# Optimization experiments

Measured on AMD Instinct MI355X. Metric: run time of the kernel, lower is better.

Reference implementation:

```python
import jax, jax.numpy as jnp
import numpy as np

D = 8
W = 256
NUM_FREQS = 10
NUM_FREQS_VIEWS = 4
SKIPS = (4,)
PE_DIM = 3 + 2 * 3 * NUM_FREQS        # 63
VE_DIM = 3 + 2 * 3 * NUM_FREQS_VIEWS  # 27
N_RAYS, N_SAMPLES = 4096, 64


def embed(x, num_freqs):
    # torch order: [x, sin(x*f0), cos(x*f0), sin(x*f1), cos(x*f1), ...]
    freqs = (2.0 ** jnp.arange(num_freqs)).astype(x.dtype)
    xf = x[..., None, :] * freqs[:, None]              # [..., F, 3]
    sc = jnp.stack([jnp.sin(xf), jnp.cos(xf)], axis=-2)  # [..., F, 2, 3]
    return jnp.concatenate([x, sc.reshape(*x.shape[:-1], num_freqs * 6)], -1)


def setup_inputs() -> dict:
    key = jax.random.key(0)
    ks = iter(jax.random.split(key, 32))
    inp = {}
    inp["input_pts"] = jax.random.normal(next(ks), (N_RAYS, N_SAMPLES, 3), jnp.float32)
    inp["input_views"] = jax.random.normal(next(ks), (N_RAYS, 3), jnp.float32)
    # pts MLP: layer 5 (index 5) takes W + PE_DIM due to skip after layer 4
    in_dims = [PE_DIM] + [(W + PE_DIM) if i in SKIPS else W for i in range(D - 1)]
    for i, d in enumerate(in_dims):
        inp[f"pts_w{i}"] = jax.random.normal(next(ks), (d, W), jnp.float32) / np.sqrt(d).astype(np.float32)
        inp[f"pts_b{i}"] = jnp.zeros((W,), jnp.float32)
    inp["views_w"] = jax.random.normal(next(ks), (VE_DIM + W, W // 2), jnp.float32) / np.sqrt(VE_DIM + W).astype(np.float32)
    inp["views_b"] = jnp.zeros((W // 2,), jnp.float32)
    inp["feat_w"] = jax.random.normal(next(ks), (W, W), jnp.float32) / np.sqrt(W).astype(np.float32)
    inp["feat_b"] = jnp.zeros((W,), jnp.float32)
    inp["alpha_w"] = jax.random.normal(next(ks), (W, 1), jnp.float32) / np.sqrt(W).astype(np.float32)
    inp["alpha_b"] = jnp.zeros((1,), jnp.float32)
    inp["rgb_w"] = jax.random.normal(next(ks), (W // 2, 3), jnp.float32) / np.sqrt(W // 2).astype(np.float32)
    inp["rgb_b"] = jnp.zeros((3,), jnp.float32)
    return inp


def reference(input_pts, input_views,
              pts_w0, pts_b0, pts_w1, pts_b1, pts_w2, pts_b2, pts_w3, pts_b3,
              pts_w4, pts_b4, pts_w5, pts_b5, pts_w6, pts_b6, pts_w7, pts_b7,
              views_w, views_b, feat_w, feat_b, alpha_w, alpha_b, rgb_w, rgb_b):
    pts_ws = [pts_w0, pts_w1, pts_w2, pts_w3, pts_w4, pts_w5, pts_w6, pts_w7]
    pts_bs = [pts_b0, pts_b1, pts_b2, pts_b3, pts_b4, pts_b5, pts_b6, pts_b7]
    R, S = input_pts.shape[0], input_pts.shape[1]
    ep = embed(input_pts, NUM_FREQS).reshape(-1, PE_DIM)            # [R*S, 63]
    ev = embed(input_views, NUM_FREQS_VIEWS)                        # [R, 27]
    ev = jnp.broadcast_to(ev[:, None, :], (R, S, VE_DIM)).reshape(-1, VE_DIM)
    h = ep
    for i in range(D):
        h = jax.nn.relu(h @ pts_ws[i] + pts_bs[i])
        if i in SKIPS:
            h = jnp.concatenate([ep, h], -1)
    alpha = h @ alpha_w + alpha_b                                    # [R*S, 1]
    feature = h @ feat_w + feat_b                                    # [R*S, W]
    h2 = jax.nn.relu(jnp.concatenate([feature, ev], -1) @ views_w + views_b)
    rgb = h2 @ rgb_w + rgb_b                                         # [R*S, 3]
    return jnp.concatenate([rgb, alpha], -1).reshape(R, S, 4)
```

## Files before the change

kernel.cpp:

```cpp
#include <hip/hip_runtime.h>

typedef _Float16 h16;
typedef __attribute__((ext_vector_type(8))) _Float16 half8;
typedef __attribute__((ext_vector_type(4))) _Float16 half4;
typedef __attribute__((ext_vector_type(4))) float f32x4;
typedef __attribute__((ext_vector_type(16))) float f32x16;

#define LDH 264
#define LDE 72

constexpr size_t OFF_P0 = 0;
constexpr size_t OFF_P1 = 16384;
constexpr size_t OFF_P2 = 81920;
constexpr size_t OFF_P3 = 147456;
constexpr size_t OFF_P4 = 212992;
constexpr size_t OFF_P5 = 278528;
constexpr size_t OFF_P6 = 360448;
constexpr size_t OFF_P7 = 425984;
constexpr size_t OFF_FEAT = 491520;
constexpr size_t OFF_VIEWS = 557056;

__device__ __forceinline__ f32x16 mfma32(half8 a, half8 b, f32x16 c) {
  return __builtin_amdgcn_mfma_f32_32x32x16_f16(a, b, c, 0, 0, 0);
}

__global__ void convw_kernel(const float* __restrict__ src, h16* __restrict__ dst,
                             int Ksrc, int N, int Kp, int p, int npad) {
  int t = blockIdx.x * 256 + threadIdx.x;
  int nfrags = (Kp >> 4) * (N >> 5);
  int frag = t >> 6;
  if (frag >= nfrags) return;
  int l = t & 63;
  int ntiles = N >> 5;
  int kt = frag / ntiles;
  int nt = frag - kt * ntiles;
  int col = nt * 32 + (l & 31);
  int kbase = kt * 16 + (l >> 5) * 8;
  half8 v;
#pragma unroll
  for (int j = 0; j < 8; ++j) {
    int k = kbase + j;
    float x = 0.f;
    if (k < p) {
      x = src[(size_t)k * N + col];
    } else if (k >= p + npad) {
      int r = k - npad;
      if (r < Ksrc) x = src[(size_t)r * N + col];
    }
    v[j] = (h16)x;
  }
  *(half8*)(dst + (size_t)frag * 512 + (size_t)l * 8) = v;
}

struct Params {
  const float* pts;
  const float* views;
  const h16* wf;
  const float* pb[8];
  const float* views_b;
  const float* feat_b;
  const float* alpha_w;
  const float* alpha_b;
  const float* rgb_w;
  const float* rgb_b;
  float* out;
};

template <int KT, int KT0, bool RELU, bool PRE_BAR>
__device__ __forceinline__ void gemm256(const h16* __restrict__ src0, int ld0,
                                        const h16* __restrict__ src1, int ld1,
                                        const h16* __restrict__ wf,
                                        const float* __restrict__ bias,
                                        h16* __restrict__ dst,
                                        int w, int l) {
  const int lr = l & 31;
  const int lk = (l >> 5) * 8;
  f32x16 acc[2];
  acc[0] = (f32x16)0.f;
  acc[1] = (f32x16)0.f;

#pragma unroll
  for (int kt = 0; kt < KT; ++kt) {
    half8 a[2];
#pragma unroll
    for (int mt = 0; mt < 2; ++mt) {
      const h16* ap;
      if (kt < KT0) ap = src0 + (size_t)(mt * 32 + lr) * ld0 + kt * 16 + lk;
      else          ap = src1 + (size_t)(mt * 32 + lr) * ld1 + (kt - KT0) * 16 + lk;
      a[mt] = *(const half8*)ap;
    }
    half8 b = *(const half8*)(wf + ((size_t)(kt * 8 + w) * 64 + l) * 8);
#pragma unroll
    for (int mt = 0; mt < 2; ++mt)
      acc[mt] = mfma32(b, a[mt], acc[mt]);
  }
  if (PRE_BAR) __syncthreads();
#pragma unroll
  for (int mt = 0; mt < 2; ++mt) {
    int row = mt * 32 + lr;
#pragma unroll
    for (int g = 0; g < 4; ++g) {
      int n0 = w * 32 + g * 8 + (l >> 5) * 4;
      f32x4 bv = *(const f32x4*)(bias + n0);
      half4 pk;
#pragma unroll
      for (int i = 0; i < 4; ++i) {
        float v = acc[mt][g * 4 + i] + bv[i];
        if (RELU) v = fmaxf(v, 0.f);
        pk[i] = (h16)v;
      }
      *(half4*)(dst + (size_t)row * LDH + n0) = pk;
    }
  }
  __syncthreads();
}

__global__ __launch_bounds__(512, 4) void nerf_kernel(Params P) {
  __shared__ __align__(16) h16 ep[64 * LDE];
  __shared__ __align__(16) h16 h[64 * LDH];
  __shared__ __align__(16) h16 evp[32];
  __shared__ float alpha_s[64];

  const int tid = threadIdx.x;
  const int w = tid >> 6, l = tid & 63;
  const int lr = l & 31;
  const int lk = (l >> 5) * 8;
  const int ray = blockIdx.x;

  if (tid < 64) {
    const int s = tid;
    const float x0 = P.pts[((size_t)ray * 64 + s) * 3 + 0];
    const float x1 = P.pts[((size_t)ray * 64 + s) * 3 + 1];
    const float x2 = P.pts[((size_t)ray * 64 + s) * 3 + 2];
    h16* e = ep + (size_t)s * LDE;
    e[0] = (h16)x0; e[1] = (h16)x1; e[2] = (h16)x2;
#pragma unroll
    for (int f = 0; f < 10; ++f) {
      const float sc = (float)(1 << f);
      e[3 + 6 * f + 0] = (h16)sinf(x0 * sc);
      e[3 + 6 * f + 1] = (h16)sinf(x1 * sc);
      e[3 + 6 * f + 2] = (h16)sinf(x2 * sc);
      e[3 + 6 * f + 3] = (h16)cosf(x0 * sc);
      e[3 + 6 * f + 4] = (h16)cosf(x1 * sc);
      e[3 + 6 * f + 5] = (h16)cosf(x2 * sc);
    }
    e[63] = (h16)0.f;
  } else if (tid < 96) {
    const int idx = tid - 64;
    float v = 0.f;
    if (idx < 27) {
      if (idx < 3) {
        v = P.views[(size_t)ray * 3 + idx];
      } else {
        const int f = (idx - 3) / 6, rem = (idx - 3) % 6, d = rem % 3;
        const float x = P.views[(size_t)ray * 3 + d] * (float)(1 << f);
        v = (rem < 3) ? sinf(x) : cosf(x);
      }
    }
    evp[idx] = (h16)v;
  }
  __syncthreads();

  gemm256<4, 4, true, false>(ep, LDE, ep, LDE, P.wf + OFF_P0, P.pb[0], h, w, l);
  gemm256<16, 0, true, true>(ep, LDE, h, LDH, P.wf + OFF_P1, P.pb[1], h, w, l);
  gemm256<16, 0, true, true>(ep, LDE, h, LDH, P.wf + OFF_P2, P.pb[2], h, w, l);
  gemm256<16, 0, true, true>(ep, LDE, h, LDH, P.wf + OFF_P3, P.pb[3], h, w, l);
  gemm256<16, 0, true, true>(ep, LDE, h, LDH, P.wf + OFF_P4, P.pb[4], h, w, l);
  gemm256<20, 4, true, true>(ep, LDE, h, LDH, P.wf + OFF_P5, P.pb[5], h, w, l);
  gemm256<16, 0, true, true>(ep, LDE, h, LDH, P.wf + OFF_P6, P.pb[6], h, w, l);
  gemm256<16, 0, true, true>(ep, LDE, h, LDH, P.wf + OFF_P7, P.pb[7], h, w, l);

  if (tid < 256) {
    const int s = tid >> 2, q = tid & 3;
    float sum = 0.f;
#pragma unroll 8
    for (int k = 0; k < 64; ++k)
      sum += (float)h[(size_t)s * LDH + q * 64 + k] * P.alpha_w[q * 64 + k];
    sum += __shfl_xor(sum, 1);
    sum += __shfl_xor(sum, 2);
    if (q == 0) alpha_s[s] = sum + P.alpha_b[0];
  }

  gemm256<16, 0, false, true>(ep, LDE, h, LDH, P.wf + OFF_FEAT, P.feat_b, h, w, l);

  {
    f32x16 acc[2];
    acc[0] = (f32x16)0.f;
    acc[1] = (f32x16)0.f;
    if (w < 4) {
#pragma unroll
      for (int kt = 0; kt < 18; ++kt) {
        half8 a[2];
        if (kt < 16) {
#pragma unroll
          for (int mt = 0; mt < 2; ++mt)
            a[mt] = *(const half8*)(h + (size_t)(mt * 32 + lr) * LDH + kt * 16 + lk);
        } else {
          half8 av = *(const half8*)(evp + (kt - 16) * 16 + lk);
          a[0] = av; a[1] = av;
        }
        half8 b = *(const half8*)(P.wf + OFF_VIEWS + ((size_t)(kt * 4 + w) * 64 + l) * 8);
#pragma unroll
        for (int mt = 0; mt < 2; ++mt)
          acc[mt] = mfma32(b, a[mt], acc[mt]);
      }
    }
    __syncthreads();
    if (w < 4) {
#pragma unroll
      for (int mt = 0; mt < 2; ++mt) {
        int row = mt * 32 + lr;
#pragma unroll
        for (int g = 0; g < 4; ++g) {
          int n0 = w * 32 + g * 8 + (l >> 5) * 4;
          f32x4 bv = *(const f32x4*)(P.views_b + n0);
          half4 pk;
#pragma unroll
          for (int i = 0; i < 4; ++i)
            pk[i] = (h16)fmaxf(acc[mt][g * 4 + i] + bv[i], 0.f);
          *(half4*)(h + (size_t)row * LDH + n0) = pk;
        }
      }
    }
    __syncthreads();
  }

  if (tid < 256) {
    const int s = tid >> 2, q = tid & 3;
    float r0 = 0.f, r1 = 0.f, r2 = 0.f;
#pragma unroll 8
    for (int k = 0; k < 32; ++k) {
      const int kk = q * 32 + k;
      const float hv = (float)h[(size_t)s * LDH + kk];
      r0 += hv * P.rgb_w[kk * 3 + 0];
      r1 += hv * P.rgb_w[kk * 3 + 1];
      r2 += hv * P.rgb_w[kk * 3 + 2];
    }
    r0 += __shfl_xor(r0, 1); r0 += __shfl_xor(r0, 2);
    r1 += __shfl_xor(r1, 1); r1 += __shfl_xor(r1, 2);
    r2 += __shfl_xor(r2, 1); r2 += __shfl_xor(r2, 2);
    if (q == 0) {
      float4 o;
      o.x = r0 + P.rgb_b[0];
      o.y = r1 + P.rgb_b[1];
      o.z = r2 + P.rgb_b[2];
      o.w = alpha_s[s];
      *(float4*)(P.out + ((size_t)ray * 64 + s) * 4) = o;
    }
  }
}

extern "C" void kernel_launch(void* const* d_in, const int* in_sizes, int n_in,
                              void* d_out, int out_size, void* d_ws, size_t ws_size,
                              hipStream_t stream) {
  h16* wsw = (h16*)d_ws;
  auto conv = [&](int idx, int Ksrc, int N, int Kp, int p, int npad, size_t off) {
    int nfrags = (Kp / 16) * (N / 32);
    int total = nfrags * 64;
    convw_kernel<<<(total + 255) / 256, 256, 0, stream>>>(
        (const float*)d_in[idx], wsw + off, Ksrc, N, Kp, p, npad);
  };
  conv(2, 63, 256, 64, 63, 1, OFF_P0);
  conv(4, 256, 256, 256, 256, 0, OFF_P1);
  conv(6, 256, 256, 256, 256, 0, OFF_P2);
  conv(8, 256, 256, 256, 256, 0, OFF_P3);
  conv(10, 256, 256, 256, 256, 0, OFF_P4);
  conv(12, 319, 256, 320, 63, 1, OFF_P5);
  conv(14, 256, 256, 256, 256, 0, OFF_P6);
  conv(16, 256, 256, 256, 256, 0, OFF_P7);
  conv(20, 256, 256, 256, 256, 0, OFF_FEAT);
  conv(18, 283, 128, 288, 283, 5, OFF_VIEWS);

  Params P;
  P.pts = (const float*)d_in[0];
  P.views = (const float*)d_in[1];
  P.wf = wsw;
  for (int i = 0; i < 8; ++i) P.pb[i] = (const float*)d_in[3 + 2 * i];
  P.views_b = (const float*)d_in[19];
  P.feat_b = (const float*)d_in[21];
  P.alpha_w = (const float*)d_in[22];
  P.alpha_b = (const float*)d_in[23];
  P.rgb_w = (const float*)d_in[24];
  P.rgb_b = (const float*)d_in[25];
  P.out = (float*)d_out;

  nerf_kernel<<<4096, 512, 0, stream>>>(P);
}
```

Baseline: 383.4 us.

## Prefetch next-layer weights into registers and double-buffer activations in LDS

Restructures the per-ray MLP so each wave keeps its weight fragments in registers and prefetches the next layer's first half of weights while computing the current layer. Activations ping-pong between two LDS buffers, which removes the pre-epilogue barrier. The skip-layer weights are rotated so the embedding part comes last. The positional embedding is spread across all 512 threads, and the views layer is split over all 8 waves instead of 4. The cost is much higher register pressure and more LDS, which may reduce occupancy at the 4-blocks launch bound.

New measurement: 388.3 us. About the same (+1.3%).

```diff
diff --git a/kernel.cpp b/kernel.cpp
--- a/kernel.cpp
+++ b/kernel.cpp
@@ -24,8 +24,12 @@
   return __builtin_amdgcn_mfma_f32_32x32x16_f16(a, b, c, 0, 0, 0);
 }
 
+__device__ __forceinline__ half8 ldfrag(const h16* __restrict__ base, int frag, int l) {
+  return *(const half8*)(base + (size_t)frag * 512 + (size_t)l * 8);
+}
+
 __global__ void convw_kernel(const float* __restrict__ src, h16* __restrict__ dst,
-                             int Ksrc, int N, int Kp, int p, int npad) {
+                             int Ksrc, int N, int Kp, int p, int npad, int rot) {
   int t = blockIdx.x * 256 + threadIdx.x;
   int nfrags = (Kp >> 4) * (N >> 5);
   int frag = t >> 6;
@@ -39,12 +43,13 @@
   half8 v;
 #pragma unroll
   for (int j = 0; j < 8; ++j) {
-    int k = kbase + j;
+    int pr = kbase + j + rot;
+    if (pr >= Kp) pr -= Kp;
     float x = 0.f;
-    if (k < p) {
-      x = src[(size_t)k * N + col];
-    } else if (k >= p + npad) {
-      int r = k - npad;
+    if (pr < p) {
+      x = src[(size_t)pr * N + col];
+    } else if (pr >= p + npad) {
+      int r = pr - npad;
       if (r < Ksrc) x = src[(size_t)r * N + col];
     }
     v[j] = (h16)x;
@@ -66,87 +71,117 @@
   float* out;
 };
 
-template <int KT, int KT0, bool RELU, bool PRE_BAR>
-__device__ __forceinline__ void gemm256(const h16* __restrict__ src0, int ld0,
-                                        const h16* __restrict__ src1, int ld1,
-                                        const h16* __restrict__ wf,
-                                        const float* __restrict__ bias,
-                                        h16* __restrict__ dst,
-                                        int w, int l) {
-  const int lr = l & 31;
-  const int lk = (l >> 5) * 8;
-  f32x16 acc[2];
-  acc[0] = (f32x16)0.f;
-  acc[1] = (f32x16)0.f;
-
-#pragma unroll
-  for (int kt = 0; kt < KT; ++kt) {
-    half8 a[2];
-#pragma unroll
-    for (int mt = 0; mt < 2; ++mt) {
-      const h16* ap;
-      if (kt < KT0) ap = src0 + (size_t)(mt * 32 + lr) * ld0 + kt * 16 + lk;
-      else          ap = src1 + (size_t)(mt * 32 + lr) * ld1 + (kt - KT0) * 16 + lk;
-      a[mt] = *(const half8*)ap;
-    }
-    half8 b = *(const half8*)(wf + ((size_t)(kt * 8 + w) * 64 + l) * 8);
-#pragma unroll
-    for (int mt = 0; mt < 2; ++mt)
-      acc[mt] = mfma32(b, a[mt], acc[mt]);
-  }
-  if (PRE_BAR) __syncthreads();
+template <bool RELU>
+__device__ __forceinline__ void epi(const f32x16& a0, const f32x16& a1,
+                                    const float* __restrict__ bias,
+                                    h16* __restrict__ Y, int w, int l, int lr) {
 #pragma unroll
   for (int mt = 0; mt < 2; ++mt) {
+    const f32x16& A = mt ? a1 : a0;
     int row = mt * 32 + lr;
 #pragma unroll
     for (int g = 0; g < 4; ++g) {
-      int n0 = w * 32 + g * 8 + (l >> 5) * 4;
+      int n0 = w * 32 + g * 8 + ((l >> 5) * 4);
       f32x4 bv = *(const f32x4*)(bias + n0);
       half4 pk;
 #pragma unroll
       for (int i = 0; i < 4; ++i) {
-        float v = acc[mt][g * 4 + i] + bv[i];
+        float v = A[g * 4 + i] + bv[i];
         if (RELU) v = fmaxf(v, 0.f);
         pk[i] = (h16)v;
       }
-      *(half4*)(dst + (size_t)row * LDH + n0) = pk;
-    }
-  }
+      *(half4*)(Y + (size_t)row * LDH + n0) = pk;
+    }
+  }
+}
+
+template <bool RELU, bool EXTEP>
+__device__ __forceinline__ void layer256(
+    const h16* __restrict__ X, const h16* __restrict__ EPb, h16* __restrict__ Y,
+    const h16* __restrict__ wcur, const h16* __restrict__ wnext,
+    int nstride, int nbase, const float* __restrict__ bias,
+    half8 (&bf)[8], half8 (&bt)[8], int w, int l, int lr, int lko) {
+#pragma unroll
+  for (int j = 0; j < 8; ++j) bt[j] = ldfrag(wcur, (8 + j) * 8 + w, l);
+  half8 bep[4];
+  f32x16 acc0 = (f32x16)0.f, acc1 = (f32x16)0.f;
+#pragma unroll
+  for (int kt = 0; kt < 16; ++kt) {
+    half8 a = *(const half8*)(X + (size_t)lr * LDH + kt * 16 + lko);
+    half8 b = kt < 8 ? bf[kt] : bt[kt - 8];
+    acc0 = mfma32(b, a, acc0);
+    if (EXTEP && kt == 7) {
+#pragma unroll
+      for (int j = 0; j < 4; ++j) bep[j] = ldfrag(wcur, (16 + j) * 8 + w, l);
+    }
+  }
+  if (EXTEP) {
+#pragma unroll
+    for (int j = 0; j < 4; ++j) {
+      half8 a = *(const half8*)(EPb + (size_t)lr * LDE + j * 16 + lko);
+      acc0 = mfma32(bep[j], a, acc0);
+    }
+  }
+#pragma unroll
+  for (int kt = 0; kt < 16; ++kt) {
+    half8 a = *(const half8*)(X + (size_t)(32 + lr) * LDH + kt * 16 + lko);
+    half8 b = kt < 8 ? bf[kt] : bt[kt - 8];
+    acc1 = mfma32(b, a, acc1);
+    if (kt < 8) bf[kt] = ldfrag(wnext, kt * nstride + nbase, l);
+  }
+  if (EXTEP) {
+#pragma unroll
+    for (int j = 0; j < 4; ++j) {
+      half8 a = *(const half8*)(EPb + (size_t)(32 + lr) * LDE + j * 16 + lko);
+      acc1 = mfma32(bep[j], a, acc1);
+    }
+  }
+  epi<RELU>(acc0, acc1, bias, Y, w, l, lr);
   __syncthreads();
 }
 
 __global__ __launch_bounds__(512, 4) void nerf_kernel(Params P) {
   __shared__ __align__(16) h16 ep[64 * LDE];
-  __shared__ __align__(16) h16 h[64 * LDH];
+  __shared__ __align__(16) h16 h0[64 * LDH];
+  __shared__ __align__(16) h16 h1[64 * LDH];
   __shared__ __align__(16) h16 evp[32];
-  __shared__ float alpha_s[64];
 
   const int tid = threadIdx.x;
   const int w = tid >> 6, l = tid & 63;
   const int lr = l & 31;
-  const int lk = (l >> 5) * 8;
+  const int lko = (l >> 5) * 8;
   const int ray = blockIdx.x;
-
-  if (tid < 64) {
-    const int s = tid;
-    const float x0 = P.pts[((size_t)ray * 64 + s) * 3 + 0];
-    const float x1 = P.pts[((size_t)ray * 64 + s) * 3 + 1];
-    const float x2 = P.pts[((size_t)ray * 64 + s) * 3 + 2];
-    h16* e = ep + (size_t)s * LDE;
-    e[0] = (h16)x0; e[1] = (h16)x1; e[2] = (h16)x2;
-#pragma unroll
-    for (int f = 0; f < 10; ++f) {
-      const float sc = (float)(1 << f);
-      e[3 + 6 * f + 0] = (h16)sinf(x0 * sc);
-      e[3 + 6 * f + 1] = (h16)sinf(x1 * sc);
-      e[3 + 6 * f + 2] = (h16)sinf(x2 * sc);
-      e[3 + 6 * f + 3] = (h16)cosf(x0 * sc);
-      e[3 + 6 * f + 4] = (h16)cosf(x1 * sc);
-      e[3 + 6 * f + 5] = (h16)cosf(x2 * sc);
-    }
-    e[63] = (h16)0.f;
-  } else if (tid < 96) {
-    const int idx = tid - 64;
+  const h16* wf = P.wf;
+
+  half8 bt[8];
+#pragma unroll
+  for (int j = 0; j < 4; ++j) bt[j] = ldfrag(wf + OFF_P0, j * 8 + w, l);
+
+  {
+    const int s = tid >> 3, q = tid & 7;
+    const float* ps = P.pts + ((size_t)ray * 64 + s) * 3;
+    const float x0 = ps[0], x1 = ps[1], x2 = ps[2];
+    half8 v;
+#pragma unroll
+    for (int j = 0; j < 8; ++j) {
+      int p = q * 8 + j;
+      float val;
+      if (p < 3) {
+        val = p == 0 ? x0 : (p == 1 ? x1 : x2);
+      } else if (p < 63) {
+        int t = p - 3;
+        int f = t / 6, rem = t % 6, d = rem % 3;
+        float x = (d == 0 ? x0 : (d == 1 ? x1 : x2)) * (float)(1 << f);
+        val = (rem < 3) ? sinf(x) : cosf(x);
+      } else {
+        val = 0.f;
+      }
+      v[j] = (h16)val;
+    }
+    *(half8*)(ep + (size_t)s * LDE + q * 8) = v;
+  }
+  if (tid < 32) {
+    const int idx = tid;
     float v = 0.f;
     if (idx < 27) {
       if (idx < 3) {
@@ -161,90 +196,114 @@
   }
   __syncthreads();
 
-  gemm256<4, 4, true, false>(ep, LDE, ep, LDE, P.wf + OFF_P0, P.pb[0], h, w, l);
-  gemm256<16, 0, true, true>(ep, LDE, h, LDH, P.wf + OFF_P1, P.pb[1], h, w, l);
-  gemm256<16, 0, true, true>(ep, LDE, h, LDH, P.wf + OFF_P2, P.pb[2], h, w, l);
-  gemm256<16, 0, true, true>(ep, LDE, h, LDH, P.wf + OFF_P3, P.pb[3], h, w, l);
-  gemm256<16, 0, true, true>(ep, LDE, h, LDH, P.wf + OFF_P4, P.pb[4], h, w, l);
-  gemm256<20, 4, true, true>(ep, LDE, h, LDH, P.wf + OFF_P5, P.pb[5], h, w, l);
-  gemm256<16, 0, true, true>(ep, LDE, h, LDH, P.wf + OFF_P6, P.pb[6], h, w, l);
-  gemm256<16, 0, true, true>(ep, LDE, h, LDH, P.wf + OFF_P7, P.pb[7], h, w, l);
-
-  if (tid < 256) {
-    const int s = tid >> 2, q = tid & 3;
+  half8 bf[8];
+
+  {
+    f32x16 acc0 = (f32x16)0.f, acc1 = (f32x16)0.f;
+#pragma unroll
+    for (int kt = 0; kt < 4; ++kt) {
+      half8 a = *(const half8*)(ep + (size_t)lr * LDE + kt * 16 + lko);
+      acc0 = mfma32(bt[kt], a, acc0);
+    }
+#pragma unroll
+    for (int kt = 0; kt < 4; ++kt) {
+      half8 a = *(const half8*)(ep + (size_t)(32 + lr) * LDE + kt * 16 + lko);
+      acc1 = mfma32(bt[kt], a, acc1);
+    }
+#pragma unroll
+    for (int j = 0; j < 8; ++j) bf[j] = ldfrag(wf + OFF_P1, j * 8 + w, l);
+    epi<true>(acc0, acc1, P.pb[0], h0, w, l, lr);
+    __syncthreads();
+  }
+
+  layer256<true, false>(h0, ep, h1, wf + OFF_P1, wf + OFF_P2, 8, w, P.pb[1], bf, bt, w, l, lr, lko);
+  layer256<true, false>(h1, ep, h0, wf + OFF_P2, wf + OFF_P3, 8, w, P.pb[2], bf, bt, w, l, lr, lko);
+  layer256<true, false>(h0, ep, h1, wf + OFF_P3, wf + OFF_P4, 8, w, P.pb[3], bf, bt, w, l, lr, lko);
+  layer256<true, false>(h1, ep, h0, wf + OFF_P4, wf + OFF_P5, 8, w, P.pb[4], bf, bt, w, l, lr, lko);
+  layer256<true, true>(h0, ep, h1, wf + OFF_P5, wf + OFF_P6, 8, w, P.pb[5], bf, bt, w, l, lr, lko);
+  layer256<true, false>(h1, ep, h0, wf + OFF_P6, wf + OFF_P7, 8, w, P.pb[6], bf, bt, w, l, lr, lko);
+  layer256<true, false>(h0, ep, h1, wf + OFF_P7, wf + OFF_FEAT, 8, w, P.pb[7], bf, bt, w, l, lr, lko);
+
+  float alpha_reg;
+  {
+    const int s = tid >> 3, q = tid & 7;
     float sum = 0.f;
-#pragma unroll 8
-    for (int k = 0; k < 64; ++k)
-      sum += (float)h[(size_t)s * LDH + q * 64 + k] * P.alpha_w[q * 64 + k];
+#pragma unroll
+    for (int j = 0; j < 4; ++j) {
+      half8 hv = *(const half8*)(h1 + (size_t)s * LDH + q * 32 + j * 8);
+#pragma unroll
+      for (int i = 0; i < 8; ++i)
+        sum += (float)hv[i] * P.alpha_w[q * 32 + j * 8 + i];
+    }
     sum += __shfl_xor(sum, 1);
     sum += __shfl_xor(sum, 2);
-    if (q == 0) alpha_s[s] = sum + P.alpha_b[0];
-  }
-
-  gemm256<16, 0, false, true>(ep, LDE, h, LDH, P.wf + OFF_FEAT, P.feat_b, h, w, l);
-
-  {
-    f32x16 acc[2];
-    acc[0] = (f32x16)0.f;
-    acc[1] = (f32x16)0.f;
-    if (w < 4) {
-#pragma unroll
-      for (int kt = 0; kt < 18; ++kt) {
-        half8 a[2];
-        if (kt < 16) {
-#pragma unroll
-          for (int mt = 0; mt < 2; ++mt)
-            a[mt] = *(const half8*)(h + (size_t)(mt * 32 + lr) * LDH + kt * 16 + lk);
-        } else {
-          half8 av = *(const half8*)(evp + (kt - 16) * 16 + lk);
-          a[0] = av; a[1] = av;
-        }
-        half8 b = *(const half8*)(P.wf + OFF_VIEWS + ((size_t)(kt * 4 + w) * 64 + l) * 8);
-#pragma unroll
-        for (int mt = 0; mt < 2; ++mt)
-          acc[mt] = mfma32(b, a[mt], acc[mt]);
-      }
+    sum += __shfl_xor(sum, 4);
+    alpha_reg = sum + P.alpha_b[0];
+  }
+
+  layer256<false, false>(h1, ep, h0, wf + OFF_FEAT, wf + OFF_VIEWS, 4, (w >> 1),
+                         P.feat_b, bf, bt, w, l, lr, lko);
+
+  {
+    const int r = w & 1, c = w >> 1;
+    const h16* wV = wf + OFF_VIEWS;
+#pragma unroll
+    for (int j = 0; j < 8; ++j) bt[j] = ldfrag(wV, (8 + j) * 4 + c, l);
+    half8 bev[2];
+    f32x16 acc = (f32x16)0.f;
+#pragma unroll
+    for (int kt = 0; kt < 16; ++kt) {
+      half8 a = *(const half8*)(h0 + (size_t)(r * 32 + lr) * LDH + kt * 16 + lko);
+      half8 b = kt < 8 ? bf[kt] : bt[kt - 8];
+      acc = mfma32(b, a, acc);
+      if (kt == 7) {
+        bev[0] = ldfrag(wV, 16 * 4 + c, l);
+        bev[1] = ldfrag(wV, 17 * 4 + c, l);
+      }
+    }
+#pragma unroll
+    for (int j = 0; j < 2; ++j) {
+      half8 a = *(const half8*)(evp + j * 16 + lko);
+      acc = mfma32(bev[j], a, acc);
+    }
+    const int row = r * 32 + lr;
+#pragma unroll
+    for (int g = 0; g < 4; ++g) {
+      int n0 = c * 32 + g * 8 + ((l >> 5) * 4);
+      f32x4 bv = *(const f32x4*)(P.views_b + n0);
+      half4 pk;
+#pragma unroll
+      for (int i = 0; i < 4; ++i)
+        pk[i] = (h16)fmaxf(acc[g * 4 + i] + bv[i], 0.f);
+      *(half4*)(h1 + (size_t)row * LDH + n0) = pk;
     }
     __syncthreads();
-    if (w < 4) {
-#pragma unroll
-      for (int mt = 0; mt < 2; ++mt) {
-        int row = mt * 32 + lr;
-#pragma unroll
-        for (int g = 0; g < 4; ++g) {
-          int n0 = w * 32 + g * 8 + (l >> 5) * 4;
-          f32x4 bv = *(const f32x4*)(P.views_b + n0);
-          half4 pk;
-#pragma unroll
-          for (int i = 0; i < 4; ++i)
-            pk[i] = (h16)fmaxf(acc[mt][g * 4 + i] + bv[i], 0.f);
-          *(half4*)(h + (size_t)row * LDH + n0) = pk;
-        }
-      }
-    }
-    __syncthreads();
-  }
-
-  if (tid < 256) {
-    const int s = tid >> 2, q = tid & 3;
+  }
+
+  {
+    const int s = tid >> 3, q = tid & 7;
     float r0 = 0.f, r1 = 0.f, r2 = 0.f;
-#pragma unroll 8
-    for (int k = 0; k < 32; ++k) {
-      const int kk = q * 32 + k;
-      const float hv = (float)h[(size_t)s * LDH + kk];
-      r0 += hv * P.rgb_w[kk * 3 + 0];
-      r1 += hv * P.rgb_w[kk * 3 + 1];
-      r2 += hv * P.rgb_w[kk * 3 + 2];
-    }
-    r0 += __shfl_xor(r0, 1); r0 += __shfl_xor(r0, 2);
-    r1 += __shfl_xor(r1, 1); r1 += __shfl_xor(r1, 2);
-    r2 += __shfl_xor(r2, 1); r2 += __shfl_xor(r2, 2);
+#pragma unroll
+    for (int j = 0; j < 2; ++j) {
+      half8 hv = *(const half8*)(h1 + (size_t)s * LDH + q * 16 + j * 8);
+#pragma unroll
+      for (int i = 0; i < 8; ++i) {
+        const int kk = q * 16 + j * 8 + i;
+        const float f = (float)hv[i];
+        r0 += f * P.rgb_w[kk * 3 + 0];
+        r1 += f * P.rgb_w[kk * 3 + 1];
+        r2 += f * P.rgb_w[kk * 3 + 2];
+      }
+    }
+    r0 += __shfl_xor(r0, 1); r0 += __shfl_xor(r0, 2); r0 += __shfl_xor(r0, 4);
+    r1 += __shfl_xor(r1, 1); r1 += __shfl_xor(r1, 2); r1 += __shfl_xor(r1, 4);
+    r2 += __shfl_xor(r2, 1); r2 += __shfl_xor(r2, 2); r2 += __shfl_xor(r2, 4);
     if (q == 0) {
       float4 o;
       o.x = r0 + P.rgb_b[0];
       o.y = r1 + P.rgb_b[1];
       o.z = r2 + P.rgb_b[2];
-      o.w = alpha_s[s];
+      o.w = alpha_reg;
       *(float4*)(P.out + ((size_t)ray * 64 + s) * 4) = o;
     }
   }
@@ -254,22 +313,22 @@
                               void* d_out, int out_size, void* d_ws, size_t ws_size,
                               hipStream_t stream) {
   h16* wsw = (h16*)d_ws;
-  auto conv = [&](int idx, int Ksrc, int N, int Kp, int p, int npad, size_t off) {
+  auto conv = [&](int idx, int Ksrc, int N, int Kp, int p, int npad, int rot, size_t off) {
     int nfrags = (Kp / 16) * (N / 32);
     int total = nfrags * 64;
     convw_kernel<<<(total + 255) / 256, 256, 0, stream>>>(
-        (const float*)d_in[idx], wsw + off, Ksrc, N, Kp, p, npad);
+        (const float*)d_in[idx], wsw + off, Ksrc, N, Kp, p, npad, rot);
   };
-  conv(2, 63, 256, 64, 63, 1, OFF_P0);
-  conv(4, 256, 256, 256, 256, 0, OFF_P1);
-  conv(6, 256, 256, 256, 256, 0, OFF_P2);
-  conv(8, 256, 256, 256, 256, 0, OFF_P3);
-  conv(10, 256, 256, 256, 256, 0, OFF_P4);
-  conv(12, 319, 256, 320, 63, 1, OFF_P5);
-  conv(14, 256, 256, 256, 256, 0, OFF_P6);
-  conv(16, 256, 256, 256, 256, 0, OFF_P7);
-  conv(20, 256, 256, 256, 256, 0, OFF_FEAT);
-  conv(18, 283, 128, 288, 283, 5, OFF_VIEWS);
+  conv(2, 63, 256, 64, 63, 1, 0, OFF_P0);
+  conv(4, 256, 256, 256, 256, 0, 0, OFF_P1);
+  conv(6, 256, 256, 256, 256, 0, 0, OFF_P2);
+  conv(8, 256, 256, 256, 256, 0, 0, OFF_P3);
+  conv(10, 256, 256, 256, 256, 0, 0, OFF_P4);
+  conv(12, 319, 256, 320, 63, 1, 64, OFF_P5);
+  conv(14, 256, 256, 256, 256, 0, 0, OFF_P6);
+  conv(16, 256, 256, 256, 256, 0, 0, OFF_P7);
+  conv(20, 256, 256, 256, 256, 0, 0, OFF_FEAT);
+  conv(18, 283, 128, 288, 283, 5, 0, OFF_VIEWS);
 
   Params P;
   P.pts = (const float*)d_in[0];
```
